# Optimization experiments

Hardware: AMD Instinct MI355X
Metric: run time of the kernel (lower is better)

The kernel has to match this reference:

```python
import jax, jax.numpy as jnp
import numpy as np

T, N = 20, 32768          # seq_length, numNodes
D_IN, D_EMB, D_H, D_OUT = 2, 64, 128, 5


def setup_inputs() -> dict:
    key = jax.random.key(0)
    ks = jax.random.split(key, 12)
    s = 0.05
    return {
        "nodes": jax.random.normal(ks[0], (T, N, D_IN), jnp.float32),
        "present_mask": jax.random.randint(ks[1], (T, N), 0, 2).astype(bool),
        "hidden_states": jax.random.normal(ks[2], (N, D_H), jnp.float32),
        "cell_states": jax.random.normal(ks[3], (N, D_H), jnp.float32),
        "W_embed": jax.random.normal(ks[4], (D_IN, D_EMB), jnp.float32) * s,
        "b_embed": jnp.zeros((D_EMB,), jnp.float32),
        "W_ih": jax.random.normal(ks[5], (D_EMB, 4 * D_H), jnp.float32) * s,
        "b_ih": jnp.zeros((4 * D_H,), jnp.float32),
        "W_hh": jax.random.normal(ks[6], (D_H, 4 * D_H), jnp.float32) * s,
        "b_hh": jnp.zeros((4 * D_H,), jnp.float32),
        "W_out": jax.random.normal(ks[7], (D_H, D_OUT), jnp.float32) * s,
        "b_out": jnp.zeros((D_OUT,), jnp.float32),
    }


def reference(nodes, present_mask, hidden_states, cell_states,
              W_embed, b_embed, W_ih, b_ih, W_hh, b_hh, W_out, b_out):
    # Per-frame: gather present nodes -> embed+ReLU (dropout=eval identity)
    # -> LSTMCell -> scatter h/c/output back. Gather+scatter is expressed as
    # a masked update, which is mathematically identical.
    def step(carry, frame):
        h, c = carry
        x, mask = frame                      # x: [N,2], mask: [N]
        emb = jax.nn.relu(x @ W_embed + b_embed)              # [N,Demb]
        gates = emb @ W_ih + b_ih + h @ W_hh + b_hh           # [N,4H]
        i, f, g, o = jnp.split(gates, 4, axis=-1)             # torch order
        i, f, o = jax.nn.sigmoid(i), jax.nn.sigmoid(f), jax.nn.sigmoid(o)
        g = jnp.tanh(g)
        c_new = f * c + i * g
        h_new = o * jnp.tanh(c_new)
        m = mask[:, None]
        h = jnp.where(m, h_new, h)
        c = jnp.where(m, c_new, c)
        out = jnp.where(m, h_new @ W_out + b_out, 0.0)        # absent -> zeros
        return (h, c), out

    (h_fin, c_fin), outputs = jax.lax.scan(
        step, (hidden_states, cell_states), (nodes, present_mask))
    return outputs, h_fin, c_fin                              # [T,N,5],[N,H],[N,H]
```

## Files before the change

kernel.cpp:

```cpp
#include <hip/hip_runtime.h>
#include <cstddef>


typedef __attribute__((ext_vector_type(8))) short  s16x8;
typedef __attribute__((ext_vector_type(4))) float  f32x4;

namespace {
constexpr int T_STEPS = 20;
constexpr int NN      = 32768;
constexpr int D_EMB   = 64;
constexpr int D_H     = 128;
constexpr int D_OUT   = 5;
constexpr int G4      = 512;
constexpr int MT      = 128;
constexpr int BLOCK   = 512;
constexpr int GRID    = NN / MT;
constexpr int RT_N    = MT / 16;
constexpr int WP_ELEMS   = 8 * 4 * 6 * 64 * 8;
constexpr int WOUT_ELEMS = 4 * 64 * 8;
constexpr int A_ELEMS    = RT_N * 6 * 64 * 8;
constexpr float LOG2E = 1.4426950408889634f;
constexpr float AM4   = -4.0f * LOG2E;
constexpr float AP2   =  2.0f * LOG2E;
constexpr float CINV  = 0.34657359027997264f;
constexpr size_t OFF_H = (size_t)T_STEPS * NN * D_OUT;
constexpr size_t OFF_C = OFF_H + (size_t)NN * D_H;
}

__device__ __forceinline__ unsigned short f2bf(float x) {
    unsigned u = __float_as_uint(x);
    u = (u + 0x7FFFu + ((u >> 16) & 1u)) >> 16;
    return (unsigned short)u;
}
__device__ __forceinline__ unsigned short f2bf_hw(float x) {
    __bf16 b = (__bf16)x;
    union { __bf16 b; unsigned short u; } cv;
    cv.b = b;
    return cv.u;
}
__device__ __forceinline__ float bf2f(unsigned short h) {
    return __uint_as_float(((unsigned)h) << 16);
}
__device__ __forceinline__ float exp2f_fast(float x) {
#if __has_builtin(__builtin_amdgcn_exp2f)
    return __builtin_amdgcn_exp2f(x);
#else
    return __expf(x * 0.6931471805599453f);
#endif
}
__device__ __forceinline__ float sig_pre(float a) {
    return __builtin_amdgcn_rcpf(1.0f + exp2f_fast(a));
}

__global__ void prepack_kernel(const float* __restrict__ W_ih,
                               const float* __restrict__ b_ih,
                               const float* __restrict__ W_hh,
                               const float* __restrict__ b_hh,
                               const float* __restrict__ W_out,
                               unsigned short* __restrict__ Wp,
                               unsigned short* __restrict__ WoutF,
                               float* __restrict__ b_sum) {
    int idx = blockIdx.x * blockDim.x + threadIdx.x;
    if (idx < WP_ELEMS) {
        int j    = idx & 7;
        int L    = (idx >> 3) & 63;
        int rest = idx >> 9;
        int kb   = rest % 6;
        int gw   = rest / 6;
        int g    = gw & 3, w = gw >> 2;
        int k    = kb * 32 + (L >> 4) * 8 + j;
        int col  = g * D_H + w * 16 + (L & 15);
        float v  = (k < D_EMB) ? W_ih[k * G4 + col] : W_hh[(k - D_EMB) * G4 + col];
        float s  = (g == 2) ? (2.0f * LOG2E) : (-LOG2E);
        Wp[idx] = f2bf(v * s);
    } else if (idx < WP_ELEMS + WOUT_ELEMS) {
        int i2 = idx - WP_ELEMS;
        int j = i2 & 7, L = (i2 >> 3) & 63, kb2 = i2 >> 9;
        int k = kb2 * 32 + (L >> 4) * 8 + j;
        int n = L & 15;
        WoutF[i2] = (n < D_OUT) ? f2bf(W_out[k * D_OUT + n]) : (unsigned short)0;
    }
    if (idx < G4) {
        int g = idx / D_H;
        float s = (g == 2) ? (2.0f * LOG2E) : (-LOG2E);
        b_sum[idx] = (b_ih[idx] + b_hh[idx]) * s;
    }
}

__global__ __launch_bounds__(BLOCK, 2) void vlstm_kernel(
    const float* __restrict__ nodes,
    const int*   __restrict__ mask,
    const float* __restrict__ h0,
    const float* __restrict__ c0,
    const float* __restrict__ W_embed,
    const float* __restrict__ b_embed,
    const float* __restrict__ b_out,
    const unsigned short* __restrict__ Wp,
    const unsigned short* __restrict__ WoutF,
    const float* __restrict__ b_sum,
    float* __restrict__ out)
{
    __shared__ __align__(16) unsigned short A[2][A_ELEMS];
    __shared__ __align__(16) unsigned short WoS[WOUT_ELEMS];
    __shared__ float We_s[2 * D_EMB];
    __shared__ float be_s[D_EMB];
    __shared__ __align__(16) unsigned long long msk64[2][2];

    const int tid  = threadIdx.x;
    const int wave = tid >> 6;
    const int L    = tid & 63;
    const int quad = L >> 4;
    const int l15  = L & 15;
    const int n_base = blockIdx.x * MT;

    const unsigned short* wbase = Wp + (size_t)wave * (4 * 6 * 64 * 8);
    s16x8 Bf[4][6];
    #pragma unroll
    for (int g = 0; g < 4; g++)
        #pragma unroll
        for (int kb = 0; kb < 6; kb++)
            Bf[g][kb] = *(const s16x8*)(wbase + ((g * 6 + kb) * 64 + L) * 8);

    const int u_lane = wave * 16 + l15;
    float bias[4];
    #pragma unroll
    for (int g = 0; g < 4; g++) bias[g] = b_sum[g * D_H + u_lane];
    const float bo = (l15 < D_OUT) ? b_out[l15] : 0.0f;

    const int kb_u = 2 + (u_lane >> 5);
    const int fl   = ((u_lane >> 3) & 3) * 16 + quad * 4;
    const int j_u  = u_lane & 7;

    for (int i = tid; i < 3 * D_EMB; i += BLOCK) {
        if (i < 2 * D_EMB) We_s[i] = W_embed[i];
        else               be_s[i - 2 * D_EMB] = b_embed[i - 2 * D_EMB];
    }
    for (int i = tid; i < WOUT_ELEMS; i += BLOCK) WoS[i] = WoutF[i];

    float          cL[RT_N][4];
    unsigned short hr[RT_N][4];
    #pragma unroll
    for (int rt = 0; rt < RT_N; rt++)
        #pragma unroll
        for (int r = 0; r < 4; r++) {
            int m = rt * 16 + quad * 4 + r;
            cL[rt][r] = AP2 * c0[(size_t)(n_base + m) * D_H + u_lane];
            hr[rt][r] = f2bf_hw(h0[(size_t)(n_base + m) * D_H + u_lane]);
            A[0][((rt * 6 + kb_u) * 64 + fl + r) * 8 + j_u] = hr[rt][r];
        }

    const int node_e = tid >> 2;
    const int eb2    = tid & 3;
    int idx_e[2];
    #pragma unroll
    for (int s = 0; s < 2; s++) {
        int e0 = eb2 * 16 + s * 8;
        idx_e[s] = (((node_e >> 4) * 6 + (e0 >> 5)) * 64 +
                    ((e0 >> 3) & 3) * 16 + (node_e & 15)) * 8;
    }

#define EMB_WRITE(AW, XV) do {                                                 \
    _Pragma("unroll")                                                          \
    for (int s = 0; s < 2; s++) {                                              \
        s16x8 ev;                                                              \
        _Pragma("unroll")                                                      \
        for (int j = 0; j < 8; j++) {                                          \
            int e = eb2 * 16 + s * 8 + j;                                      \
            float v = fmaf((XV).x, We_s[e], fmaf((XV).y, We_s[D_EMB + e], be_s[e])); \
            ev[j] = (short)f2bf_hw(fmaxf(v, 0.0f));                            \
        }                                                                      \
        *(s16x8*)((AW) + idx_e[s]) = ev;                                       \
    } } while (0)

    {
        float2 x0 = *(const float2*)(nodes + (size_t)(n_base + node_e) * 2);
        EMB_WRITE(A[0], x0);
        int lm0 = (tid < MT) ? mask[n_base + tid] : 0;
        if (wave < 2) {
            unsigned long long bm = __ballot(lm0 != 0);
            if (L == 0) msk64[0][wave] = bm;
        }
    }
    __syncthreads();

#define GEMM_RT(rt) do {                                                       \
    {   s16x8 af0 = *(const s16x8*)(Ar + (((rt) * 6 + 0) * 64 + L) * 8);       \
        _Pragma("unroll")                                                      \
        for (int g = 0; g < 4; g++)                                            \
            acc[(rt) & 1][g] = __builtin_amdgcn_mfma_f32_16x16x32_bf16(        \
                af0, Bf[g][0], (f32x4){0.f, 0.f, 0.f, 0.f}, 0, 0, 0); }        \
    _Pragma("unroll")                                                          \
    for (int kb = 1; kb < 6; kb++) {                                           \
        s16x8 af = *(const s16x8*)(Ar + (((rt) * 6 + kb) * 64 + L) * 8);       \
        _Pragma("unroll")                                                      \
        for (int g = 0; g < 4; g++)                                            \
            acc[(rt) & 1][g] = __builtin_amdgcn_mfma_f32_16x16x32_bf16(        \
                af, Bf[g][kb], acc[(rt) & 1][g], 0, 0, 0); }                   \
} while (0)

#define ACT_RT(rt, MW) do {                                                    \
    unsigned nib = (unsigned)((MW) >> (((rt) & 3) * 16 + quad * 4)) & 0xFu;    \
    _Pragma("unroll")                                                          \
    for (int r = 0; r < 4; r++) {                                              \
        float gi = sig_pre(acc[(rt) & 1][0][r] + bias[0]);                     \
        float gf = sig_pre(acc[(rt) & 1][1][r] + bias[1]);                     \
        float rg = sig_pre(acc[(rt) & 1][2][r] + bias[2]);                     \
        float go = sig_pre(acc[(rt) & 1][3][r] + bias[3]);                     \
        float ggL = fmaf(AM4, rg, AP2);                   \
        float cnL = fmaf(gf, cL[rt][r], gi * ggL);        \
        float rr  = __builtin_amdgcn_rcpf(1.0f + exp2f_fast(cnL));             \
        float hv  = go * fmaf(-2.0f, rr, 1.0f);           \
        unsigned short hb = f2bf_hw(hv);                                       \
        if ((nib >> r) & 1u) { cL[rt][r] = cnL; hr[rt][r] = hb; }              \
        Aw[(((rt) * 6 + kb_u) * 64 + fl + r) * 8 + j_u] = hr[rt][r];           \
    } } while (0)

#define OPROJ(ARP, TIDX, MPA, MPB) do {                                        \
    f32x4 ao = (f32x4){0.f, 0.f, 0.f, 0.f};                                    \
    _Pragma("unroll")                                                          \
    for (int kb2 = 0; kb2 < 4; kb2++) {                                        \
        s16x8 af = *(const s16x8*)((ARP) + ((wave * 6 + 2 + kb2) * 64 + L) * 8); \
        s16x8 wf = *(const s16x8*)(WoS + (kb2 * 64 + L) * 8);                  \
        ao = __builtin_amdgcn_mfma_f32_16x16x32_bf16(af, wf, ao, 0, 0, 0);     \
    }                                                                          \
    if (l15 < D_OUT) {                                                         \
        unsigned long long Mw = (wave < 4) ? (MPA) : (MPB);                    \
        unsigned nib = (unsigned)(Mw >> ((wave & 3) * 16 + quad * 4)) & 0xFu;  \
        float* ob = out + ((size_t)(TIDX) * NN + n_base) * D_OUT + l15;        \
        _Pragma("unroll")                                                      \
        for (int r = 0; r < 4; r++) {                                          \
            int node = wave * 16 + quad * 4 + r;                               \
            ob[node * D_OUT] = ((nib >> r) & 1u) ? (ao[r] + bo) : 0.0f;        \
        }                                                                      \
    } } while (0)

    unsigned long long Mp0 = 0, Mp1 = 0;

    for (int t = 0; t < T_STEPS; t++) {
        unsigned short* __restrict__ Ar = A[t & 1];
        unsigned short* __restrict__ Aw = A[(t + 1) & 1];

        const unsigned long long M0 = msk64[t & 1][0];
        const unsigned long long M1 = msk64[t & 1][1];

        float2 xv = make_float2(0.0f, 0.0f);
        int    lm = 0;
        if (t + 1 < T_STEPS) {
            xv = *(const float2*)(nodes + ((size_t)(t + 1) * NN + n_base + node_e) * 2);
            if (tid < MT) lm = mask[(size_t)(t + 1) * NN + n_base + tid];
        }

        f32x4 acc[2][4];
        GEMM_RT(0);
        GEMM_RT(1);
        ACT_RT(0, M0);
        GEMM_RT(2);
        ACT_RT(1, M0);
        GEMM_RT(3);
        ACT_RT(2, M0);
        if (t > 0) OPROJ(Ar, t - 1, Mp0, Mp1);
        ACT_RT(3, M0);
        GEMM_RT(4);
        GEMM_RT(5);
        ACT_RT(4, M1);
        GEMM_RT(6);
        ACT_RT(5, M1);
        GEMM_RT(7);
        ACT_RT(6, M1);
        if (t + 1 < T_STEPS) {
            EMB_WRITE(Aw, xv);
            if (wave < 2) {
                unsigned long long bm = __ballot(lm != 0);
                if (L == 0) msk64[(t + 1) & 1][wave] = bm;
            }
        }
        ACT_RT(7, M1);

        Mp0 = M0; Mp1 = M1;
        __syncthreads();
    }

    OPROJ(A[0], T_STEPS - 1, Mp0, Mp1);

    for (int i = tid; i < MT * D_H; i += BLOCK) {
        int node = i >> 7, u = i & 127;
        int idx = (((node >> 4) * 6 + 2 + (u >> 5)) * 64 +
                   ((u >> 3) & 3) * 16 + (node & 15)) * 8 + (u & 7);
        out[OFF_H + (size_t)(n_base + node) * D_H + u] = bf2f(A[0][idx]);
    }

    __syncthreads();
    float* cs = (float*)A;
    #pragma unroll
    for (int rt = 0; rt < RT_N; rt++)
        #pragma unroll
        for (int r = 0; r < 4; r++) {
            int m = rt * 16 + quad * 4 + r;
            cs[m * 129 + u_lane] = CINV * cL[rt][r];
        }
    __syncthreads();
    for (int i = tid; i < MT * D_H; i += BLOCK) {
        int node = i >> 7, u = i & 127;
        out[OFF_C + (size_t)(n_base + node) * D_H + u] = cs[node * 129 + u];
    }

#undef EMB_WRITE
#undef GEMM_RT
#undef ACT_RT
#undef OPROJ
}

extern "C" void kernel_launch(void* const* d_in, const int* in_sizes, int n_in,
                              void* d_out, int out_size, void* d_ws, size_t ws_size,
                              hipStream_t stream) {
    const float* nodes   = (const float*)d_in[0];
    const int*   mask    = (const int*)  d_in[1];
    const float* h0      = (const float*)d_in[2];
    const float* c0      = (const float*)d_in[3];
    const float* W_embed = (const float*)d_in[4];
    const float* b_embed = (const float*)d_in[5];
    const float* W_ih    = (const float*)d_in[6];
    const float* b_ih    = (const float*)d_in[7];
    const float* W_hh    = (const float*)d_in[8];
    const float* b_hh    = (const float*)d_in[9];
    const float* W_out   = (const float*)d_in[10];
    const float* b_out   = (const float*)d_in[11];
    float* out = (float*)d_out;

    unsigned short* Wp    = (unsigned short*)d_ws;
    unsigned short* WoutF = Wp + WP_ELEMS;
    float*          b_sum = (float*)(WoutF + WOUT_ELEMS);

    prepack_kernel<<<(WP_ELEMS + WOUT_ELEMS + 255) / 256, 256, 0, stream>>>(
        W_ih, b_ih, W_hh, b_hh, W_out, Wp, WoutF, b_sum);

    vlstm_kernel<<<GRID, BLOCK, 0, stream>>>(
        nodes, mask, h0, c0, W_embed, b_embed, b_out, Wp, WoutF, b_sum, out);
}
```

Baseline: 279.9 us.

## Halve node tile, stream weights from global, and split gates into two passes

Shrinks the per-block node tile from 128 to 64 and raises the launch-bounds occupancy target from 2 to 4 blocks per CU. Weight fragments are no longer held in registers for the whole kernel but reloaded from global (L2) memory every timestep. Gate computation is split into two passes (i,g then f,o) to cut accumulator register pressure. The aim is higher occupancy and better latency hiding, paid for with repeated weight reads each step, twice as many blocks, and a changed embed and mask layout.

Result: slower. 751.1 us (+168.3%).

```diff
diff --git a/kernel.cpp b/kernel.cpp
--- a/kernel.cpp
+++ b/kernel.cpp
@@ -12,7 +12,7 @@
 constexpr int D_H     = 128;
 constexpr int D_OUT   = 5;
 constexpr int G4      = 512;
-constexpr int MT      = 128;
+constexpr int MT      = 64;
 constexpr int BLOCK   = 512;
 constexpr int GRID    = NN / MT;
 constexpr int RT_N    = MT / 16;
@@ -87,7 +87,7 @@
     }
 }
 
-__global__ __launch_bounds__(BLOCK, 2) void vlstm_kernel(
+__global__ __launch_bounds__(BLOCK, 4) void vlstm_kernel(
     const float* __restrict__ nodes,
     const int*   __restrict__ mask,
     const float* __restrict__ h0,
@@ -104,7 +104,7 @@
     __shared__ __align__(16) unsigned short WoS[WOUT_ELEMS];
     __shared__ float We_s[2 * D_EMB];
     __shared__ float be_s[D_EMB];
-    __shared__ __align__(16) unsigned long long msk64[2][2];
+    __shared__ unsigned long long msk64[2];
 
     const int tid  = threadIdx.x;
     const int wave = tid >> 6;
@@ -113,13 +113,7 @@
     const int l15  = L & 15;
     const int n_base = blockIdx.x * MT;
 
-    const unsigned short* wbase = Wp + (size_t)wave * (4 * 6 * 64 * 8);
-    s16x8 Bf[4][6];
-    #pragma unroll
-    for (int g = 0; g < 4; g++)
-        #pragma unroll
-        for (int kb = 0; kb < 6; kb++)
-            Bf[g][kb] = *(const s16x8*)(wbase + ((g * 6 + kb) * 64 + L) * 8);
+    const unsigned short* __restrict__ wbase = Wp + (size_t)wave * (4 * 6 * 64 * 8);
 
     const int u_lane = wave * 16 + l15;
     float bias[4];
@@ -149,73 +143,56 @@
             A[0][((rt * 6 + kb_u) * 64 + fl + r) * 8 + j_u] = hr[rt][r];
         }
 
-    const int node_e = tid >> 2;
-    const int eb2    = tid & 3;
-    int idx_e[2];
-    #pragma unroll
-    for (int s = 0; s < 2; s++) {
-        int e0 = eb2 * 16 + s * 8;
-        idx_e[s] = (((node_e >> 4) * 6 + (e0 >> 5)) * 64 +
-                    ((e0 >> 3) & 3) * 16 + (node_e & 15)) * 8;
-    }
+    const int node_e = tid >> 3;
+    const int eb     = tid & 7;
+    const int idx_e  = (((node_e >> 4) * 6 + (eb >> 2)) * 64 + (eb & 3) * 16 + (node_e & 15)) * 8;
 
 #define EMB_WRITE(AW, XV) do {                                                 \
+    s16x8 ev;                                                                  \
     _Pragma("unroll")                                                          \
-    for (int s = 0; s < 2; s++) {                                              \
-        s16x8 ev;                                                              \
-        _Pragma("unroll")                                                      \
-        for (int j = 0; j < 8; j++) {                                          \
-            int e = eb2 * 16 + s * 8 + j;                                      \
-            float v = fmaf((XV).x, We_s[e], fmaf((XV).y, We_s[D_EMB + e], be_s[e])); \
-            ev[j] = (short)f2bf_hw(fmaxf(v, 0.0f));                            \
-        }                                                                      \
-        *(s16x8*)((AW) + idx_e[s]) = ev;                                       \
-    } } while (0)
+    for (int j = 0; j < 8; j++) {                                              \
+        int e = eb * 8 + j;                                                    \
+        float v = fmaf((XV).x, We_s[e], fmaf((XV).y, We_s[D_EMB + e], be_s[e])); \
+        ev[j] = (short)f2bf_hw(fmaxf(v, 0.0f));                                \
+    }                                                                          \
+    *(s16x8*)((AW) + idx_e) = ev;                                              \
+} while (0)
 
     {
         float2 x0 = *(const float2*)(nodes + (size_t)(n_base + node_e) * 2);
         EMB_WRITE(A[0], x0);
-        int lm0 = (tid < MT) ? mask[n_base + tid] : 0;
-        if (wave < 2) {
-            unsigned long long bm = __ballot(lm0 != 0);
-            if (L == 0) msk64[0][wave] = bm;
+        if (wave == 0) {
+            int lm0 = mask[n_base + L];
+            unsigned long long bm0 = __ballot(lm0 != 0);
+            if (L == 0) msk64[0] = bm0;
         }
     }
     __syncthreads();
 
-#define GEMM_RT(rt) do {                                                       \
-    {   s16x8 af0 = *(const s16x8*)(Ar + (((rt) * 6 + 0) * 64 + L) * 8);       \
+#define PASS(GA, GB) do {                                                      \
+    _Pragma("unroll")                                                          \
+    for (int kb = 0; kb < 6; kb++) {                                           \
+        s16x8 ba = *(const s16x8*)(wbase + (((GA) * 6 + kb) * 64 + L) * 8);    \
+        s16x8 bb = *(const s16x8*)(wbase + (((GB) * 6 + kb) * 64 + L) * 8);    \
         _Pragma("unroll")                                                      \
-        for (int g = 0; g < 4; g++)                                            \
-            acc[(rt) & 1][g] = __builtin_amdgcn_mfma_f32_16x16x32_bf16(        \
-                af0, Bf[g][0], (f32x4){0.f, 0.f, 0.f, 0.f}, 0, 0, 0); }        \
-    _Pragma("unroll")                                                          \
-    for (int kb = 1; kb < 6; kb++) {                                           \
-        s16x8 af = *(const s16x8*)(Ar + (((rt) * 6 + kb) * 64 + L) * 8);       \
-        _Pragma("unroll")                                                      \
-        for (int g = 0; g < 4; g++)                                            \
-            acc[(rt) & 1][g] = __builtin_amdgcn_mfma_f32_16x16x32_bf16(        \
-                af, Bf[g][kb], acc[(rt) & 1][g], 0, 0, 0); }                   \
+        for (int rt = 0; rt < RT_N; rt++) {                                    \
+            s16x8 af = *(const s16x8*)(Ar + ((rt * 6 + kb) * 64 + L) * 8);     \
+            if (kb == 0) {                                                     \
+                acc[rt][0] = __builtin_amdgcn_mfma_f32_16x16x32_bf16(          \
+                    af, ba, (f32x4){0.f, 0.f, 0.f, 0.f}, 0, 0, 0);             \
+                acc[rt][1] = __builtin_amdgcn_mfma_f32_16x16x32_bf16(          \
+                    af, bb, (f32x4){0.f, 0.f, 0.f, 0.f}, 0, 0, 0);             \
+            } else {                                                           \
+                acc[rt][0] = __builtin_amdgcn_mfma_f32_16x16x32_bf16(          \
+                    af, ba, acc[rt][0], 0, 0, 0);                              \
+                acc[rt][1] = __builtin_amdgcn_mfma_f32_16x16x32_bf16(          \
+                    af, bb, acc[rt][1], 0, 0, 0);                              \
+            }                                                                  \
+        }                                                                      \
+    }                                                                          \
 } while (0)
 
-#define ACT_RT(rt, MW) do {                                                    \
-    unsigned nib = (unsigned)((MW) >> (((rt) & 3) * 16 + quad * 4)) & 0xFu;    \
-    _Pragma("unroll")                                                          \
-    for (int r = 0; r < 4; r++) {                                              \
-        float gi = sig_pre(acc[(rt) & 1][0][r] + bias[0]);                     \
-        float gf = sig_pre(acc[(rt) & 1][1][r] + bias[1]);                     \
-        float rg = sig_pre(acc[(rt) & 1][2][r] + bias[2]);                     \
-        float go = sig_pre(acc[(rt) & 1][3][r] + bias[3]);                     \
-        float ggL = fmaf(AM4, rg, AP2);                   \
-        float cnL = fmaf(gf, cL[rt][r], gi * ggL);        \
-        float rr  = __builtin_amdgcn_rcpf(1.0f + exp2f_fast(cnL));             \
-        float hv  = go * fmaf(-2.0f, rr, 1.0f);           \
-        unsigned short hb = f2bf_hw(hv);                                       \
-        if ((nib >> r) & 1u) { cL[rt][r] = cnL; hr[rt][r] = hb; }              \
-        Aw[(((rt) * 6 + kb_u) * 64 + fl + r) * 8 + j_u] = hr[rt][r];           \
-    } } while (0)
-
-#define OPROJ(ARP, TIDX, MPA, MPB) do {                                        \
+#define OPROJ(ARP, TIDX, MP) do {                                              \
     f32x4 ao = (f32x4){0.f, 0.f, 0.f, 0.f};                                    \
     _Pragma("unroll")                                                          \
     for (int kb2 = 0; kb2 < 4; kb2++) {                                        \
@@ -224,8 +201,7 @@
         ao = __builtin_amdgcn_mfma_f32_16x16x32_bf16(af, wf, ao, 0, 0, 0);     \
     }                                                                          \
     if (l15 < D_OUT) {                                                         \
-        unsigned long long Mw = (wave < 4) ? (MPA) : (MPB);                    \
-        unsigned nib = (unsigned)(Mw >> ((wave & 3) * 16 + quad * 4)) & 0xFu;  \
+        unsigned nib = (unsigned)((MP) >> (wave * 16 + quad * 4)) & 0xFu;      \
         float* ob = out + ((size_t)(TIDX) * NN + n_base) * D_OUT + l15;        \
         _Pragma("unroll")                                                      \
         for (int r = 0; r < 4; r++) {                                          \
@@ -234,53 +210,67 @@
         }                                                                      \
     } } while (0)
 
-    unsigned long long Mp0 = 0, Mp1 = 0;
+    unsigned long long Mp = 0;
 
     for (int t = 0; t < T_STEPS; t++) {
         unsigned short* __restrict__ Ar = A[t & 1];
         unsigned short* __restrict__ Aw = A[(t + 1) & 1];
-
-        const unsigned long long M0 = msk64[t & 1][0];
-        const unsigned long long M1 = msk64[t & 1][1];
+        const unsigned long long M = msk64[t & 1];
 
         float2 xv = make_float2(0.0f, 0.0f);
         int    lm = 0;
         if (t + 1 < T_STEPS) {
             xv = *(const float2*)(nodes + ((size_t)(t + 1) * NN + n_base + node_e) * 2);
-            if (tid < MT) lm = mask[(size_t)(t + 1) * NN + n_base + tid];
-        }
-
-        f32x4 acc[2][4];
-        GEMM_RT(0);
-        GEMM_RT(1);
-        ACT_RT(0, M0);
-        GEMM_RT(2);
-        ACT_RT(1, M0);
-        GEMM_RT(3);
-        ACT_RT(2, M0);
-        if (t > 0) OPROJ(Ar, t - 1, Mp0, Mp1);
-        ACT_RT(3, M0);
-        GEMM_RT(4);
-        GEMM_RT(5);
-        ACT_RT(4, M1);
-        GEMM_RT(6);
-        ACT_RT(5, M1);
-        GEMM_RT(7);
-        ACT_RT(6, M1);
+            if (wave == 0) lm = mask[(size_t)(t + 1) * NN + n_base + L];
+        }
+
+        f32x4 acc[RT_N][2];
+
+        PASS(0, 2);
+
+        float P[RT_N][4];
+        #pragma unroll
+        for (int rt = 0; rt < RT_N; rt++)
+            #pragma unroll
+            for (int r = 0; r < 4; r++) {
+                float gi = sig_pre(acc[rt][0][r] + bias[0]);
+                float rg = sig_pre(acc[rt][1][r] + bias[2]);
+                P[rt][r] = gi * fmaf(AM4, rg, AP2);
+            }
+
+        if (t > 0 && wave < 4) OPROJ(Ar, t - 1, Mp);
+
+        PASS(1, 3);
+
+        #pragma unroll
+        for (int rt = 0; rt < RT_N; rt++) {
+            unsigned nib = (unsigned)(M >> (rt * 16 + quad * 4)) & 0xFu;
+            #pragma unroll
+            for (int r = 0; r < 4; r++) {
+                float gf = sig_pre(acc[rt][0][r] + bias[1]);
+                float go = sig_pre(acc[rt][1][r] + bias[3]);
+                float cnL = fmaf(gf, cL[rt][r], P[rt][r]);
+                float rr  = __builtin_amdgcn_rcpf(1.0f + exp2f_fast(cnL));
+                float hv  = go * fmaf(-2.0f, rr, 1.0f);
+                unsigned short hb = f2bf_hw(hv);
+                if ((nib >> r) & 1u) { cL[rt][r] = cnL; hr[rt][r] = hb; }
+                Aw[((rt * 6 + kb_u) * 64 + fl + r) * 8 + j_u] = hr[rt][r];
+            }
+        }
+
         if (t + 1 < T_STEPS) {
             EMB_WRITE(Aw, xv);
-            if (wave < 2) {
+            if (wave == 0) {
                 unsigned long long bm = __ballot(lm != 0);
-                if (L == 0) msk64[(t + 1) & 1][wave] = bm;
+                if (L == 0) msk64[(t + 1) & 1] = bm;
             }
         }
-        ACT_RT(7, M1);
-
-        Mp0 = M0; Mp1 = M1;
+
+        Mp = M;
         __syncthreads();
     }
 
-    OPROJ(A[0], T_STEPS - 1, Mp0, Mp1);
+    if (wave < 4) OPROJ(A[0], T_STEPS - 1, Mp);
 
     for (int i = tid; i < MT * D_H; i += BLOCK) {
         int node = i >> 7, u = i & 127;
@@ -305,8 +295,7 @@
     }
 
 #undef EMB_WRITE
-#undef GEMM_RT
-#undef ACT_RT
+#undef PASS
 #undef OPROJ
 }
 
```

## Compact present nodes per frame so GEMM runs only on active tiles

Applied to the files above, without the earlier changes.

Each frame's mask is turned into a compacted list of present nodes with ballot and popcount. Only those rows are gathered into the MFMA input tile, so the gate GEMM and activations run only on ceil(nActive/16) row tiles instead of all of them. Cell and hidden state now live in padded shared arrays indexed by original node, and outputs are scattered back through a staging buffer. The tile shrinks to 64 nodes per block with one block per CU. The cost is extra gather/scatter work, divergent tile counts per block, and a second barrier per step.

New measurement: 272.8 us. 1.03x faster.

```diff
diff --git a/kernel.cpp b/kernel.cpp
--- a/kernel.cpp
+++ b/kernel.cpp
@@ -12,13 +12,11 @@
 constexpr int D_H     = 128;
 constexpr int D_OUT   = 5;
 constexpr int G4      = 512;
-constexpr int MT      = 128;
+constexpr int MT      = 64;
 constexpr int BLOCK   = 512;
 constexpr int GRID    = NN / MT;
-constexpr int RT_N    = MT / 16;
 constexpr int WP_ELEMS   = 8 * 4 * 6 * 64 * 8;
 constexpr int WOUT_ELEMS = 4 * 64 * 8;
-constexpr int A_ELEMS    = RT_N * 6 * 64 * 8;
 constexpr float LOG2E = 1.4426950408889634f;
 constexpr float AM4   = -4.0f * LOG2E;
 constexpr float AP2   =  2.0f * LOG2E;
@@ -87,7 +85,7 @@
     }
 }
 
-__global__ __launch_bounds__(BLOCK, 2) void vlstm_kernel(
+__global__ __launch_bounds__(BLOCK, 1) void vlstm_kernel(
     const float* __restrict__ nodes,
     const int*   __restrict__ mask,
     const float* __restrict__ h0,
@@ -100,11 +98,17 @@
     const float* __restrict__ b_sum,
     float* __restrict__ out)
 {
-    __shared__ __align__(16) unsigned short A[2][A_ELEMS];
+    __shared__ __align__(16) unsigned short Acp[2][4 * 6 * 512];
+    __shared__ __align__(16) unsigned short hNewC[2][4 * 4 * 512];
+    __shared__ float          cS[MT * 132];
+    __shared__ unsigned short hS[MT * 130];
+    __shared__ float          st_o[2][MT * D_OUT];
     __shared__ __align__(16) unsigned short WoS[WOUT_ELEMS];
     __shared__ float We_s[2 * D_EMB];
     __shared__ float be_s[D_EMB];
-    __shared__ __align__(16) unsigned long long msk64[2][2];
+    __shared__ unsigned long long msk64[2];
+    __shared__ unsigned char lst[2][MT];
+    __shared__ int nAs[2];
 
     const int tid  = threadIdx.x;
     const int wave = tid >> 6;
@@ -112,6 +116,7 @@
     const int quad = L >> 4;
     const int l15  = L & 15;
     const int n_base = blockIdx.x * MT;
+    const int u_lane = wave * 16 + l15;
 
     const unsigned short* wbase = Wp + (size_t)wave * (4 * 6 * 64 * 8);
     s16x8 Bf[4][6];
@@ -121,15 +126,17 @@
         for (int kb = 0; kb < 6; kb++)
             Bf[g][kb] = *(const s16x8*)(wbase + ((g * 6 + kb) * 64 + L) * 8);
 
-    const int u_lane = wave * 16 + l15;
     float bias[4];
     #pragma unroll
     for (int g = 0; g < 4; g++) bias[g] = b_sum[g * D_H + u_lane];
     const float bo = (l15 < D_OUT) ? b_out[l15] : 0.0f;
 
-    const int kb_u = 2 + (u_lane >> 5);
-    const int fl   = ((u_lane >> 3) & 3) * 16 + quad * 4;
+    const int kbu2 = u_lane >> 5;
+    const int flg  = ((u_lane >> 3) & 3) * 128 + (u_lane & 7);
     const int j_u  = u_lane & 7;
+    const int flh  = ((u_lane >> 3) & 3) * 128 + quad * 32;
+    const int node_e = tid >> 3;
+    const int eb     = tid & 7;
 
     for (int i = tid; i < 3 * D_EMB; i += BLOCK) {
         if (i < 2 * D_EMB) We_s[i] = W_embed[i];
@@ -137,177 +144,200 @@
     }
     for (int i = tid; i < WOUT_ELEMS; i += BLOCK) WoS[i] = WoutF[i];
 
-    float          cL[RT_N][4];
-    unsigned short hr[RT_N][4];
-    #pragma unroll
-    for (int rt = 0; rt < RT_N; rt++)
-        #pragma unroll
-        for (int r = 0; r < 4; r++) {
-            int m = rt * 16 + quad * 4 + r;
-            cL[rt][r] = AP2 * c0[(size_t)(n_base + m) * D_H + u_lane];
-            hr[rt][r] = f2bf_hw(h0[(size_t)(n_base + m) * D_H + u_lane]);
-            A[0][((rt * 6 + kb_u) * 64 + fl + r) * 8 + j_u] = hr[rt][r];
-        }
-
-    const int node_e = tid >> 2;
-    const int eb2    = tid & 3;
-    int idx_e[2];
-    #pragma unroll
-    for (int s = 0; s < 2; s++) {
-        int e0 = eb2 * 16 + s * 8;
-        idx_e[s] = (((node_e >> 4) * 6 + (e0 >> 5)) * 64 +
-                    ((e0 >> 3) & 3) * 16 + (node_e & 15)) * 8;
-    }
-
-#define EMB_WRITE(AW, XV) do {                                                 \
-    _Pragma("unroll")                                                          \
-    for (int s = 0; s < 2; s++) {                                              \
+    for (int i = tid; i < MT * D_H; i += BLOCK) {
+        int node = i >> 7, u = i & 127;
+        cS[node * 132 + u] = AP2 * c0[(size_t)(n_base + node) * D_H + u];
+        hS[node * 130 + u] = f2bf_hw(h0[(size_t)(n_base + node) * D_H + u]);
+    }
+    if (wave == 0) {
+        int lm0 = mask[n_base + L];
+        unsigned long long bm = __ballot(lm0 != 0);
+        int na     = __popcll(bm);
+        int below  = __popcll(bm & ((1ull << L) - 1ull));
+        int belowI = __popcll((~bm) & ((1ull << L) - 1ull));
+        lst[0][lm0 ? below : (na + belowI)] = (unsigned char)L;
+        if (L == 0) { msk64[0] = bm; nAs[0] = na; }
+    }
+    __syncthreads();
+
+#define EMB_BUILD(B, XV, MN) do {                                              \
+    if (((MN) >> node_e) & 1ull) {                                             \
+        int j = __popcll((MN) & ((1ull << node_e) - 1ull));                    \
         s16x8 ev;                                                              \
         _Pragma("unroll")                                                      \
-        for (int j = 0; j < 8; j++) {                                          \
-            int e = eb2 * 16 + s * 8 + j;                                      \
+        for (int jj = 0; jj < 8; jj++) {                                       \
+            int e = eb * 8 + jj;                                               \
             float v = fmaf((XV).x, We_s[e], fmaf((XV).y, We_s[D_EMB + e], be_s[e])); \
-            ev[j] = (short)f2bf_hw(fmaxf(v, 0.0f));                            \
+            ev[jj] = (short)f2bf_hw(fmaxf(v, 0.0f));                           \
         }                                                                      \
-        *(s16x8*)((AW) + idx_e[s]) = ev;                                       \
+        *(s16x8*)(&Acp[B][((j >> 4) * 6 + (eb >> 2)) * 512 + (eb & 3) * 128 + (j & 15) * 8]) = ev; \
+    } } while (0)
+
+#define GATHER(B, LP, NAN_) do {                                               \
+    for (int j = quad; j < (NAN_); j += 4) {                                   \
+        int orig = (int)(LP)[j];                                               \
+        Acp[B][((j >> 4) * 6 + 2 + kbu2) * 512 + flg + (j & 15) * 8] =         \
+            hS[orig * 130 + u_lane];                                           \
     } } while (0)
 
     {
         float2 x0 = *(const float2*)(nodes + (size_t)(n_base + node_e) * 2);
-        EMB_WRITE(A[0], x0);
-        int lm0 = (tid < MT) ? mask[n_base + tid] : 0;
-        if (wave < 2) {
-            unsigned long long bm = __ballot(lm0 != 0);
-            if (L == 0) msk64[0][wave] = bm;
-        }
+        unsigned long long M0v = msk64[0];
+        EMB_BUILD(0, x0, M0v);
+        int nA0 = __builtin_amdgcn_readfirstlane(nAs[0]);
+        GATHER(0, lst[0], nA0);
     }
     __syncthreads();
 
 #define GEMM_RT(rt) do {                                                       \
-    {   s16x8 af0 = *(const s16x8*)(Ar + (((rt) * 6 + 0) * 64 + L) * 8);       \
+    {   s16x8 af0 = *(const s16x8*)(Ar + ((rt) * 6 + 0) * 512 + L * 8);        \
         _Pragma("unroll")                                                      \
         for (int g = 0; g < 4; g++)                                            \
             acc[(rt) & 1][g] = __builtin_amdgcn_mfma_f32_16x16x32_bf16(        \
                 af0, Bf[g][0], (f32x4){0.f, 0.f, 0.f, 0.f}, 0, 0, 0); }        \
     _Pragma("unroll")                                                          \
     for (int kb = 1; kb < 6; kb++) {                                           \
-        s16x8 af = *(const s16x8*)(Ar + (((rt) * 6 + kb) * 64 + L) * 8);       \
+        s16x8 af = *(const s16x8*)(Ar + ((rt) * 6 + kb) * 512 + L * 8);        \
         _Pragma("unroll")                                                      \
         for (int g = 0; g < 4; g++)                                            \
             acc[(rt) & 1][g] = __builtin_amdgcn_mfma_f32_16x16x32_bf16(        \
                 af, Bf[g][kb], acc[(rt) & 1][g], 0, 0, 0); }                   \
 } while (0)
 
-#define ACT_RT(rt, MW) do {                                                    \
-    unsigned nib = (unsigned)((MW) >> (((rt) & 3) * 16 + quad * 4)) & 0xFu;    \
+#define ACT_RT(rt) do {                                                        \
     _Pragma("unroll")                                                          \
     for (int r = 0; r < 4; r++) {                                              \
+        int c    = (rt) * 16 + quad * 4 + r;                                   \
+        int orig = (int)lstT[c];                                               \
+        float cold = cS[orig * 132 + u_lane];                                  \
         float gi = sig_pre(acc[(rt) & 1][0][r] + bias[0]);                     \
         float gf = sig_pre(acc[(rt) & 1][1][r] + bias[1]);                     \
         float rg = sig_pre(acc[(rt) & 1][2][r] + bias[2]);                     \
         float go = sig_pre(acc[(rt) & 1][3][r] + bias[3]);                     \
         float ggL = fmaf(AM4, rg, AP2);                   \
-        float cnL = fmaf(gf, cL[rt][r], gi * ggL);        \
+        float cnL = fmaf(gf, cold, gi * ggL);             \
         float rr  = __builtin_amdgcn_rcpf(1.0f + exp2f_fast(cnL));             \
         float hv  = go * fmaf(-2.0f, rr, 1.0f);           \
         unsigned short hb = f2bf_hw(hv);                                       \
-        if ((nib >> r) & 1u) { cL[rt][r] = cnL; hr[rt][r] = hb; }              \
-        Aw[(((rt) * 6 + kb_u) * 64 + fl + r) * 8 + j_u] = hr[rt][r];           \
-    } } while (0)
-
-#define OPROJ(ARP, TIDX, MPA, MPB) do {                                        \
-    f32x4 ao = (f32x4){0.f, 0.f, 0.f, 0.f};                                    \
-    _Pragma("unroll")                                                          \
-    for (int kb2 = 0; kb2 < 4; kb2++) {                                        \
-        s16x8 af = *(const s16x8*)((ARP) + ((wave * 6 + 2 + kb2) * 64 + L) * 8); \
-        s16x8 wf = *(const s16x8*)(WoS + (kb2 * 64 + L) * 8);                  \
-        ao = __builtin_amdgcn_mfma_f32_16x16x32_bf16(af, wf, ao, 0, 0, 0);     \
-    }                                                                          \
-    if (l15 < D_OUT) {                                                         \
-        unsigned long long Mw = (wave < 4) ? (MPA) : (MPB);                    \
-        unsigned nib = (unsigned)(Mw >> ((wave & 3) * 16 + quad * 4)) & 0xFu;  \
-        float* ob = out + ((size_t)(TIDX) * NN + n_base) * D_OUT + l15;        \
-        _Pragma("unroll")                                                      \
-        for (int r = 0; r < 4; r++) {                                          \
-            int node = wave * 16 + quad * 4 + r;                               \
-            ob[node * D_OUT] = ((nib >> r) & 1u) ? (ao[r] + bo) : 0.0f;        \
+        if (c < nA) {                                                          \
+            cS[orig * 132 + u_lane] = cnL;                                     \
+            hS[orig * 130 + u_lane] = hb;                                      \
+            hNc[((rt) * 4 + kbu2) * 512 + flh + r * 8 + j_u] = hb;             \
         }                                                                      \
     } } while (0)
 
-    unsigned long long Mp0 = 0, Mp1 = 0;
+    unsigned long long Mp = 0;
+    int nAp = 0;
 
     for (int t = 0; t < T_STEPS; t++) {
-        unsigned short* __restrict__ Ar = A[t & 1];
-        unsigned short* __restrict__ Aw = A[(t + 1) & 1];
-
-        const unsigned long long M0 = msk64[t & 1][0];
-        const unsigned long long M1 = msk64[t & 1][1];
+        unsigned short* __restrict__ Ar   = Acp[t & 1];
+        unsigned short* __restrict__ hNc  = hNewC[t & 1];
+        const unsigned short* __restrict__ hPv = hNewC[(t + 1) & 1];
+        const unsigned char*  __restrict__ lstT = lst[t & 1];
+
+        const unsigned long long M = msk64[t & 1];
+        const int nA  = __builtin_amdgcn_readfirstlane(nAs[t & 1]);
+        const int ntA = (nA + 15) >> 4;
 
         float2 xv = make_float2(0.0f, 0.0f);
-        int    lm = 0;
         if (t + 1 < T_STEPS) {
             xv = *(const float2*)(nodes + ((size_t)(t + 1) * NN + n_base + node_e) * 2);
-            if (tid < MT) lm = mask[(size_t)(t + 1) * NN + n_base + tid];
+            if (wave == 0) {
+                int lm = mask[(size_t)(t + 1) * NN + n_base + L];
+                unsigned long long bm = __ballot(lm != 0);
+                int na     = __popcll(bm);
+                int below  = __popcll(bm & ((1ull << L) - 1ull));
+                int belowI = __popcll((~bm) & ((1ull << L) - 1ull));
+                lst[(t + 1) & 1][lm ? below : (na + belowI)] = (unsigned char)L;
+                if (L == 0) { msk64[(t + 1) & 1] = bm; nAs[(t + 1) & 1] = na; }
+            }
         }
 
         f32x4 acc[2][4];
-        GEMM_RT(0);
-        GEMM_RT(1);
-        ACT_RT(0, M0);
-        GEMM_RT(2);
-        ACT_RT(1, M0);
-        GEMM_RT(3);
-        ACT_RT(2, M0);
-        if (t > 0) OPROJ(Ar, t - 1, Mp0, Mp1);
-        ACT_RT(3, M0);
-        GEMM_RT(4);
-        GEMM_RT(5);
-        ACT_RT(4, M1);
-        GEMM_RT(6);
-        ACT_RT(5, M1);
-        GEMM_RT(7);
-        ACT_RT(6, M1);
+        if (ntA > 0) GEMM_RT(0);
+        if (ntA > 1) GEMM_RT(1);
+        if (ntA > 0) ACT_RT(0);
+        if (ntA > 2) GEMM_RT(2);
+        if (ntA > 1) ACT_RT(1);
+        if (ntA > 3) GEMM_RT(3);
+        if (ntA > 2) ACT_RT(2);
+        if (t > 0) {
+            int ntP = (nAp + 15) >> 4;
+            if (wave < ntP) {
+                f32x4 ao = (f32x4){0.f, 0.f, 0.f, 0.f};
+                #pragma unroll
+                for (int kb2 = 0; kb2 < 4; kb2++) {
+                    s16x8 af = *(const s16x8*)(hPv + (wave * 4 + kb2) * 512 + L * 8);
+                    s16x8 wf = *(const s16x8*)(WoS + (kb2 * 64 + L) * 8);
+                    ao = __builtin_amdgcn_mfma_f32_16x16x32_bf16(af, wf, ao, 0, 0, 0);
+                }
+                if (l15 < D_OUT) {
+                    #pragma unroll
+                    for (int r = 0; r < 4; r++) {
+                        int c = wave * 16 + quad * 4 + r;
+                        st_o[(t - 1) & 1][c * D_OUT + l15] = ao[r] + bo;
+                    }
+                }
+            }
+        }
+        if (ntA > 3) ACT_RT(3);
+        __syncthreads();
+
+        if (t > 0 && tid < MT * D_OUT) {
+            int node = tid / D_OUT, d = tid - node * D_OUT;
+            int act  = (int)((Mp >> node) & 1ull);
+            int pos  = __popcll(Mp & ((1ull << node) - 1ull));
+            float v  = act ? st_o[(t - 1) & 1][pos * D_OUT + d] : 0.0f;
+            out[((size_t)(t - 1) * NN + n_base) * D_OUT + tid] = v;
+        }
         if (t + 1 < T_STEPS) {
-            EMB_WRITE(Aw, xv);
-            if (wave < 2) {
-                unsigned long long bm = __ballot(lm != 0);
-                if (L == 0) msk64[(t + 1) & 1][wave] = bm;
+            unsigned long long Mn = msk64[(t + 1) & 1];
+            EMB_BUILD((t + 1) & 1, xv, Mn);
+            int nAn = __builtin_amdgcn_readfirstlane(nAs[(t + 1) & 1]);
+            GATHER((t + 1) & 1, lst[(t + 1) & 1], nAn);
+        }
+        Mp = M; nAp = nA;
+        __syncthreads();
+    }
+
+    {
+        int ntP = (nAp + 15) >> 4;
+        if (wave < ntP) {
+            const unsigned short* hPv = hNewC[(T_STEPS - 1) & 1];
+            f32x4 ao = (f32x4){0.f, 0.f, 0.f, 0.f};
+            #pragma unroll
+            for (int kb2 = 0; kb2 < 4; kb2++) {
+                s16x8 af = *(const s16x8*)(hPv + (wave * 4 + kb2) * 512 + L * 8);
+                s16x8 wf = *(const s16x8*)(WoS + (kb2 * 64 + L) * 8);
+                ao = __builtin_amdgcn_mfma_f32_16x16x32_bf16(af, wf, ao, 0, 0, 0);
             }
-        }
-        ACT_RT(7, M1);
-
-        Mp0 = M0; Mp1 = M1;
-        __syncthreads();
-    }
-
-    OPROJ(A[0], T_STEPS - 1, Mp0, Mp1);
-
+            if (l15 < D_OUT) {
+                #pragma unroll
+                for (int r = 0; r < 4; r++) {
+                    int c = wave * 16 + quad * 4 + r;
+                    st_o[(T_STEPS - 1) & 1][c * D_OUT + l15] = ao[r] + bo;
+                }
+            }
+        }
+    }
+    __syncthreads();
+    if (tid < MT * D_OUT) {
+        int node = tid / D_OUT, d = tid - node * D_OUT;
+        int act  = (int)((Mp >> node) & 1ull);
+        int pos  = __popcll(Mp & ((1ull << node) - 1ull));
+        float v  = act ? st_o[(T_STEPS - 1) & 1][pos * D_OUT + d] : 0.0f;
+        out[((size_t)(T_STEPS - 1) * NN + n_base) * D_OUT + tid] = v;
+    }
     for (int i = tid; i < MT * D_H; i += BLOCK) {
         int node = i >> 7, u = i & 127;
-        int idx = (((node >> 4) * 6 + 2 + (u >> 5)) * 64 +
-                   ((u >> 3) & 3) * 16 + (node & 15)) * 8 + (u & 7);
-        out[OFF_H + (size_t)(n_base + node) * D_H + u] = bf2f(A[0][idx]);
-    }
-
-    __syncthreads();
-    float* cs = (float*)A;
-    #pragma unroll
-    for (int rt = 0; rt < RT_N; rt++)
-        #pragma unroll
-        for (int r = 0; r < 4; r++) {
-            int m = rt * 16 + quad * 4 + r;
-            cs[m * 129 + u_lane] = CINV * cL[rt][r];
-        }
-    __syncthreads();
-    for (int i = tid; i < MT * D_H; i += BLOCK) {
-        int node = i >> 7, u = i & 127;
-        out[OFF_C + (size_t)(n_base + node) * D_H + u] = cs[node * 129 + u];
-    }
-
-#undef EMB_WRITE
+        out[OFF_H + (size_t)(n_base + node) * D_H + u] = bf2f(hS[node * 130 + u]);
+        out[OFF_C + (size_t)(n_base + node) * D_H + u] = CINV * cS[node * 132 + u];
+    }
+
+#undef EMB_BUILD
+#undef GATHER
 #undef GEMM_RT
 #undef ACT_RT
-#undef OPROJ
 }
 
 extern "C" void kernel_launch(void* const* d_in, const int* in_sizes, int n_in,
```
